# Kernel tuning notes

Hardware: AMD Instinct MI355X
Metric: run time of the kernel (lower is better)

Reference implementation:

```python
import jax, jax.numpy as jnp
import numpy as np

NUM_NODES = 100000
NUM_EDGES = 3200000
NUM_GRAPHS = 64


def gcn_conv(x, edge_index, W, b):
    """PyG GCNConv: add self-loops, symmetric deg normalization, linear, scatter-add."""
    n = x.shape[0]
    loop = jnp.arange(n, dtype=edge_index.dtype)
    src = jnp.concatenate([edge_index[0], loop])  # message sources
    dst = jnp.concatenate([edge_index[1], loop])  # aggregation targets
    deg = jax.ops.segment_sum(jnp.ones_like(src, dtype=x.dtype), dst, num_segments=n)
    dis = jnp.where(deg > 0, jax.lax.rsqrt(jnp.maximum(deg, 1.0)), 0.0)
    norm = dis[src] * dis[dst]  # [E+N]
    h = x @ W  # linear transform first (small dims)
    msg = h[src] * norm[:, None]  # irregular gather
    out = jax.ops.segment_sum(msg, dst, num_segments=n)  # scatter-add
    return out + b


def setup_inputs() -> dict:
    key = jax.random.key(0)
    ks = jax.random.split(key, 12)
    x = jax.random.normal(ks[0], (NUM_NODES, 3), dtype=jnp.float32)
    edge_index = jax.random.randint(ks[1], (2, NUM_EDGES), 0, NUM_NODES, dtype=jnp.int64)
    batch = jnp.sort(jax.random.randint(ks[2], (NUM_NODES,), 0, NUM_GRAPHS, dtype=jnp.int64))
    def glorot(k, fan_in, fan_out):
        s = (6.0 / (fan_in + fan_out)) ** 0.5
        return jax.random.uniform(k, (fan_in, fan_out), jnp.float32, -s, s)
    return {
        'x': x, 'edge_index': edge_index, 'batch': batch,
        'W1': glorot(ks[3], 3, 32), 'b1': jnp.zeros((32,), jnp.float32),
        'W2': glorot(ks[4], 32, 16), 'b2': jnp.zeros((16,), jnp.float32),
        'W3': glorot(ks[5], 16, 8), 'b3': jnp.zeros((8,), jnp.float32),
        'Wf': glorot(ks[6], 8, 3), 'bf': jnp.zeros((3,), jnp.float32),
    }


def reference(x, edge_index, batch, W1, b1, W2, b2, W3, b3, Wf, bf):
    h = jax.nn.relu(gcn_conv(x, edge_index, W1, b1))
    h = jax.nn.relu(gcn_conv(h, edge_index, W2, b2))
    h = jax.nn.relu(gcn_conv(h, edge_index, W3, b3))
    # global mean pool over graphs
    sums = jax.ops.segment_sum(h, batch, num_segments=NUM_GRAPHS)
    cnts = jax.ops.segment_sum(jnp.ones((h.shape[0],), h.dtype), batch, num_segments=NUM_GRAPHS)
    pooled = sums / jnp.maximum(cnts, 1.0)[:, None]
    return pooled @ Wf + bf
```

## Files before the change

kernel.cpp:

```cpp
#include <hip/hip_runtime.h>

constexpr int N_NODES  = 100000;
constexpr int N_EDGES  = 3200000;
constexpr int N_GRAPHS = 64;

constexpr int BSHIFT  = 8;
constexpr int NBINS   = (N_NODES + 255) >> BSHIFT;
constexpr int BIN_CAP = 9216;
constexpr int EPB     = 8192;
constexpr int NB_BIN  = (N_EDGES + EPB - 1) / EPB;


__global__ __launch_bounds__(1024) void bin_kernel(
        const int* __restrict__ src, const int* __restrict__ dst,
        int* __restrict__ bin_cur, int2* __restrict__ binned) {
    __shared__ int hist[NBINS];
    __shared__ int base[NBINS];
    int tid = threadIdx.x;
    int e0 = blockIdx.x * EPB;
    int e1 = min(e0 + EPB, N_EDGES);
    for (int i = tid; i < NBINS; i += 1024) hist[i] = 0;
    __syncthreads();
    for (int e = e0 + tid; e < e1; e += 1024) atomicAdd(&hist[dst[e] >> BSHIFT], 1);
    __syncthreads();
    for (int i = tid; i < NBINS; i += 1024) {
        int h = hist[i];
        base[i] = h ? atomicAdd(&bin_cur[i], h) : 0;
    }
    __syncthreads();
    for (int i = tid; i < NBINS; i += 1024) hist[i] = 0;
    __syncthreads();
    for (int e = e0 + tid; e < e1; e += 1024) {
        int d = dst[e];
        int b = d >> BSHIFT;
        int r = base[b] + atomicAdd(&hist[b], 1);
        if (r < BIN_CAP) binned[(size_t)b * BIN_CAP + r] = make_int2(src[e], d);
    }
}

__global__ void binscan_kernel(const int* __restrict__ bin_cur, int* __restrict__ bin_base,
                               int* __restrict__ rowptr) {
    __shared__ int s[512];
    int t = threadIdx.x;
    int v = (t < NBINS) ? bin_cur[t] : 0;
    s[t] = v;
    __syncthreads();
    for (int o = 1; o < 512; o <<= 1) {
        int x = (t >= o) ? s[t - o] : 0;
        __syncthreads();
        s[t] += x;
        __syncthreads();
    }
    if (t < NBINS) bin_base[t] = s[t] - v;
    if (t == 0) rowptr[N_NODES] = N_EDGES;
}

__global__ __launch_bounds__(1024) void csrbuild_kernel(
        const int2* __restrict__ binned, const int* __restrict__ bin_cur,
        const int* __restrict__ bin_base, int* __restrict__ rowptr,
        float* __restrict__ dis, int* __restrict__ csr) {
    __shared__ int cnt[256];
    __shared__ int lofs[256];
    __shared__ int s[256];
    int b = blockIdx.x;
    int t = threadIdx.x;
    int size  = min(bin_cur[b], BIN_CAP);
    int gbase = bin_base[b];
    const int2* bp = binned + (size_t)b * BIN_CAP;
    if (t < 256) cnt[t] = 0;
    __syncthreads();
    for (int i = t; i < size; i += 1024) atomicAdd(&cnt[bp[i].y & 255], 1);
    __syncthreads();
    if (t < 256) {
        int n = (b << BSHIFT) + t;
        int deg = cnt[t];
        if (n < N_NODES) dis[n] = 1.0f / sqrtf((float)deg + 1.0f);
        s[t] = deg;
    }
    __syncthreads();
    for (int o = 1; o < 256; o <<= 1) {
        int x = 0;
        if (t < 256 && t >= o) x = s[t - o];
        __syncthreads();
        if (t < 256) s[t] += x;
        __syncthreads();
    }
    if (t < 256) {
        int n = (b << BSHIFT) + t;
        int deg = cnt[t];
        int excl = s[t] - deg;
        if (n < N_NODES) rowptr[n] = gbase + excl;
        lofs[t] = excl;
        cnt[t] = 0;
    }
    __syncthreads();
    for (int i = t; i < size; i += 1024) {
        int2 ed = bp[i];
        int ln = ed.y & 255;
        int r = atomicAdd(&cnt[ln], 1);
        csr[gbase + lofs[ln] + r] = ed.x;
    }
}


__global__ void pre1_kernel(const float* __restrict__ x, const float* __restrict__ dis,
                            float* __restrict__ xs) {
    int i = blockIdx.x * blockDim.x + threadIdx.x;
    if (i >= N_NODES) return;
    float d = dis[i];
    float4 v;
    v.x = x[(size_t)i * 3 + 0] * d;
    v.y = x[(size_t)i * 3 + 1] * d;
    v.z = x[(size_t)i * 3 + 2] * d;
    v.w = 0.f;
    *reinterpret_cast<float4*>(&xs[(size_t)i * 4]) = v;
}

template<int F, bool ADD_B, bool RELU>
__global__ void gather_kernel(const float* __restrict__ in, const int* __restrict__ rowptr,
                              const int* __restrict__ csr, const float* __restrict__ dis,
                              const float* __restrict__ b, float* __restrict__ out) {
    constexpr int GPB = 256 / F;
    int tid = threadIdx.x;
    int l = tid & (F - 1);
    int n = blockIdx.x * GPB + (tid / F);
    if (n >= N_NODES) return;
    int beg = rowptr[n], end = rowptr[n + 1];
    float a0 = in[(size_t)n * F + l];
    float a1 = 0.f, a2 = 0.f, a3 = 0.f;
    int k = beg;
    for (; k + 3 < end; k += 4) {
        int s0 = csr[k], s1 = csr[k + 1], s2 = csr[k + 2], s3 = csr[k + 3];
        a0 += in[(size_t)s0 * F + l];
        a1 += in[(size_t)s1 * F + l];
        a2 += in[(size_t)s2 * F + l];
        a3 += in[(size_t)s3 * F + l];
    }
    for (; k < end; ++k) a0 += in[(size_t)csr[k] * F + l];
    float v = ((a0 + a1) + (a2 + a3)) * dis[n];
    if (ADD_B) v += b[l];
    if (RELU) v = fmaxf(v, 0.f);
    out[(size_t)n * F + l] = v;
}

__global__ void lin1_kernel(const float* __restrict__ m, const float* __restrict__ W1,
                            const float* __restrict__ b1, float* __restrict__ h1) {
    int i = blockIdx.x * blockDim.x + threadIdx.x;
    if (i >= N_NODES) return;
    float4 mv = *reinterpret_cast<const float4*>(&m[(size_t)i * 4]);
#pragma unroll
    for (int f = 0; f < 32; ++f) {
        float s = b1[f];
        s = fmaf(mv.x, W1[0 * 32 + f], s);
        s = fmaf(mv.y, W1[1 * 32 + f], s);
        s = fmaf(mv.z, W1[2 * 32 + f], s);
        h1[(size_t)i * 32 + f] = fmaxf(s, 0.f);
    }
}

template<int FIN, int FOUT>
__global__ void lin_pre_kernel(const float* __restrict__ in, const float* __restrict__ W,
                               const float* __restrict__ dis, float* __restrict__ g) {
    int i = blockIdx.x * blockDim.x + threadIdx.x;
    if (i >= N_NODES) return;
    float xin[FIN];
#pragma unroll
    for (int k = 0; k < FIN; ++k) xin[k] = in[(size_t)i * FIN + k];
    float d = dis[i];
#pragma unroll
    for (int f = 0; f < FOUT; ++f) {
        float s = 0.f;
#pragma unroll
        for (int k = 0; k < FIN; ++k) s = fmaf(xin[k], W[k * FOUT + f], s);
        g[(size_t)i * FOUT + f] = s * d;
    }
}


__global__ void pool_kernel(const float* __restrict__ h, const int* __restrict__ batch,
                            float* __restrict__ pool) {
    __shared__ float lsum[N_GRAPHS * 8];
    __shared__ float lcnt[N_GRAPHS];
    int tid = threadIdx.x;
    for (int j = tid; j < N_GRAPHS * 8; j += blockDim.x) lsum[j] = 0.f;
    for (int j = tid; j < N_GRAPHS; j += blockDim.x) lcnt[j] = 0.f;
    __syncthreads();
    int i = blockIdx.x * blockDim.x + tid;
    if (i < N_NODES) {
        int gm = batch[i];
        const float4* hp = reinterpret_cast<const float4*>(&h[(size_t)i * 8]);
        float4 a = hp[0], bq = hp[1];
        atomicAdd(&lsum[gm * 8 + 0], a.x);
        atomicAdd(&lsum[gm * 8 + 1], a.y);
        atomicAdd(&lsum[gm * 8 + 2], a.z);
        atomicAdd(&lsum[gm * 8 + 3], a.w);
        atomicAdd(&lsum[gm * 8 + 4], bq.x);
        atomicAdd(&lsum[gm * 8 + 5], bq.y);
        atomicAdd(&lsum[gm * 8 + 6], bq.z);
        atomicAdd(&lsum[gm * 8 + 7], bq.w);
        atomicAdd(&lcnt[gm], 1.0f);
    }
    __syncthreads();
    for (int idx = tid; idx < N_GRAPHS * 9; idx += blockDim.x) {
        int gm = idx / 9, j = idx % 9;
        if (lcnt[gm] != 0.f) {
            if (j < 8) atomicAdd(&pool[gm * 8 + j], lsum[gm * 8 + j]);
            else       atomicAdd(&pool[512 + gm], lcnt[gm]);
        }
    }
}

__global__ void final_kernel(const float* __restrict__ pool, const float* __restrict__ Wf,
                             const float* __restrict__ bf, float* __restrict__ out) {
    int t = threadIdx.x;
    if (t >= N_GRAPHS * 3) return;
    int gm = t / 3, c = t % 3;
    float cnt = fmaxf(pool[512 + gm], 1.0f);
    float s = 0.f;
#pragma unroll
    for (int f = 0; f < 8; ++f) s = fmaf(pool[gm * 8 + f] / cnt, Wf[f * 3 + c], s);
    out[t] = s + bf[c];
}


extern "C" void kernel_launch(void* const* d_in, const int* in_sizes, int n_in,
                              void* d_out, int out_size, void* d_ws, size_t ws_size,
                              hipStream_t stream) {
    const float* x     = (const float*)d_in[0];
    const int*   ei    = (const int*)d_in[1];
    const int*   batch = (const int*)d_in[2];
    const float* W1 = (const float*)d_in[3];
    const float* b1 = (const float*)d_in[4];
    const float* W2 = (const float*)d_in[5];
    const float* b2 = (const float*)d_in[6];
    const float* W3 = (const float*)d_in[7];
    const float* b3 = (const float*)d_in[8];
    const float* Wf = (const float*)d_in[9];
    const float* bf = (const float*)d_in[10];

    const int* src = ei;
    const int* dst = ei + N_EDGES;

    const int N = N_NODES, E = N_EDGES;

    int*   bin_cur  = (int*)d_ws;
    int*   bin_base = bin_cur + NBINS;
    int*   rowptr   = bin_base + NBINS;
    float* dis      = (float*)(rowptr + N + 2);
    int*   csr      = (int*)(dis + N);
    int2*  binned   = (int2*)(csr + E);
    float* xs       = (float*)binned;
    float* m        = xs + (size_t)4 * N;
    float* h1       = m + (size_t)4 * N;
    float* g        = h1 + (size_t)32 * N;
    float* h2       = g + (size_t)16 * N;
    float* pool     = (float*)(binned + (size_t)NBINS * BIN_CAP);
    float* h3       = xs;

    const int B = 256;
    const int NB_N = (N + B - 1) / B;

    hipMemsetAsync(bin_cur, 0, NBINS * sizeof(int), stream);
    hipMemsetAsync(pool, 0, N_GRAPHS * 9 * sizeof(float), stream);

    bin_kernel<<<NB_BIN, 1024, 0, stream>>>(src, dst, bin_cur, binned);
    binscan_kernel<<<1, 512, 0, stream>>>(bin_cur, bin_base, rowptr);
    csrbuild_kernel<<<NBINS, 1024, 0, stream>>>(binned, bin_cur, bin_base, rowptr, dis, csr);

    pre1_kernel<<<NB_N, B, 0, stream>>>(x, dis, xs);
    gather_kernel<4, false, false><<<(N + 63) / 64, B, 0, stream>>>(xs, rowptr, csr, dis, b1, m);
    lin1_kernel<<<NB_N, B, 0, stream>>>(m, W1, b1, h1);

    lin_pre_kernel<32, 16><<<NB_N, B, 0, stream>>>(h1, W2, dis, g);
    gather_kernel<16, true, true><<<(N + 15) / 16, B, 0, stream>>>(g, rowptr, csr, dis, b2, h2);

    lin_pre_kernel<16, 8><<<NB_N, B, 0, stream>>>(h2, W3, dis, g);
    gather_kernel<8, true, true><<<(N + 31) / 32, B, 0, stream>>>(g, rowptr, csr, dis, b3, h3);

    pool_kernel<<<NB_N, B, 0, stream>>>(h3, batch, pool);
    final_kernel<<<1, 256, 0, stream>>>(pool, Wf, bf, (float*)d_out);
}
```

Before: 202.9 us.

## Pack binned edges, locally sort bins in LDS, split 16-wide gather into halves

The bin kernel now stages each block's edges in shared memory and counting-sorts them by bin, so global writes to the binned buffer are contiguous per bin. Each edge is packed into one int holding the low destination bits and the source index, which halves binned traffic; csrbuild keeps these packed values in registers between its two passes. The 16-feature layer-2 gather is split into two 8-feature gathers over separate arrays, trading an extra pass over the CSR for smaller gathered rows. Nontemporal loads and stores are added throughout. The bin kernel uses a large LDS footprint, which lowers occupancy.

```diff
diff --git a/kernel.cpp b/kernel.cpp
--- a/kernel.cpp
+++ b/kernel.cpp
@@ -4,37 +4,83 @@
 constexpr int N_EDGES  = 3200000;
 constexpr int N_GRAPHS = 64;
 
-constexpr int BSHIFT  = 8;
-constexpr int NBINS   = (N_NODES + 255) >> BSHIFT;
-constexpr int BIN_CAP = 9216;
-constexpr int EPB     = 8192;
-constexpr int NB_BIN  = (N_EDGES + EPB - 1) / EPB;
+constexpr int BSHIFT   = 8;
+constexpr int NBINS    = (N_NODES + 255) >> BSHIFT;
+constexpr int BIN_CAP  = 9216;
+constexpr int SRC_BITS = 17;
+constexpr int SRC_MASK = (1 << SRC_BITS) - 1;
+
+constexpr int NB_BIN = 500;
+constexpr int EPB    = N_EDGES / NB_BIN;
+constexpr int EPT    = (EPB + 1023) / 1024;
+
+typedef float v4f __attribute__((ext_vector_type(4)));
 
 
 __global__ __launch_bounds__(1024) void bin_kernel(
         const int* __restrict__ src, const int* __restrict__ dst,
-        int* __restrict__ bin_cur, int2* __restrict__ binned) {
+        int* __restrict__ bin_cur, int* __restrict__ binned) {
+    __shared__ int pk[EPB];
+    __shared__ unsigned short bn[EPB];
+    __shared__ unsigned short ord[EPB];
     __shared__ int hist[NBINS];
-    __shared__ int base[NBINS];
+    __shared__ int lexcl[NBINS];
+    __shared__ int lofs[NBINS];
+    __shared__ int gofs[NBINS];
+    __shared__ int s512[512];
     int tid = threadIdx.x;
     int e0 = blockIdx.x * EPB;
-    int e1 = min(e0 + EPB, N_EDGES);
     for (int i = tid; i < NBINS; i += 1024) hist[i] = 0;
     __syncthreads();
-    for (int e = e0 + tid; e < e1; e += 1024) atomicAdd(&hist[dst[e] >> BSHIFT], 1);
-    __syncthreads();
-    for (int i = tid; i < NBINS; i += 1024) {
-        int h = hist[i];
-        base[i] = h ? atomicAdd(&bin_cur[i], h) : 0;
-    }
-    __syncthreads();
-    for (int i = tid; i < NBINS; i += 1024) hist[i] = 0;
-    __syncthreads();
-    for (int e = e0 + tid; e < e1; e += 1024) {
-        int d = dst[e];
-        int b = d >> BSHIFT;
-        int r = base[b] + atomicAdd(&hist[b], 1);
-        if (r < BIN_CAP) binned[(size_t)b * BIN_CAP + r] = make_int2(src[e], d);
+#pragma unroll
+    for (int k = 0; k < EPT; ++k) {
+        int i = tid + k * 1024;
+        if (i < EPB) {
+            int d = __builtin_nontemporal_load(&dst[e0 + i]);
+            int s = __builtin_nontemporal_load(&src[e0 + i]);
+            int b = d >> BSHIFT;
+            pk[i] = ((d & 255) << SRC_BITS) | s;
+            bn[i] = (unsigned short)b;
+            atomicAdd(&hist[b], 1);
+        }
+    }
+    __syncthreads();
+    if (tid < 512) s512[tid] = (tid < NBINS) ? hist[tid] : 0;
+    __syncthreads();
+    for (int o = 1; o < 512; o <<= 1) {
+        int x = 0;
+        if (tid < 512 && tid >= o) x = s512[tid - o];
+        __syncthreads();
+        if (tid < 512) s512[tid] += x;
+        __syncthreads();
+    }
+    if (tid < NBINS) {
+        int h = hist[tid];
+        int excl = s512[tid] - h;
+        lexcl[tid] = excl;
+        lofs[tid]  = excl;
+        gofs[tid]  = h ? atomicAdd(&bin_cur[tid], h) : 0;
+    }
+    __syncthreads();
+#pragma unroll
+    for (int k = 0; k < EPT; ++k) {
+        int i = tid + k * 1024;
+        if (i < EPB) {
+            int r = atomicAdd(&lofs[bn[i]], 1);
+            ord[r] = (unsigned short)i;
+        }
+    }
+    __syncthreads();
+#pragma unroll
+    for (int k = 0; k < EPT; ++k) {
+        int i = tid + k * 1024;
+        if (i < EPB) {
+            int j = ord[i];
+            int b = bn[j];
+            int pos = gofs[b] + (i - lexcl[b]);
+            if (pos < BIN_CAP)
+                __builtin_nontemporal_store(pk[j], &binned[(size_t)b * BIN_CAP + pos]);
+        }
     }
 }
 
@@ -56,7 +102,7 @@
 }
 
 __global__ __launch_bounds__(1024) void csrbuild_kernel(
-        const int2* __restrict__ binned, const int* __restrict__ bin_cur,
+        const int* __restrict__ binned, const int* __restrict__ bin_cur,
         const int* __restrict__ bin_base, int* __restrict__ rowptr,
         float* __restrict__ dis, int* __restrict__ csr) {
     __shared__ int cnt[256];
@@ -66,10 +112,16 @@
     int t = threadIdx.x;
     int size  = min(bin_cur[b], BIN_CAP);
     int gbase = bin_base[b];
-    const int2* bp = binned + (size_t)b * BIN_CAP;
+    const int* bp = binned + (size_t)b * BIN_CAP;
     if (t < 256) cnt[t] = 0;
     __syncthreads();
-    for (int i = t; i < size; i += 1024) atomicAdd(&cnt[bp[i].y & 255], 1);
+    int pc[9];
+#pragma unroll
+    for (int k = 0; k < 9; ++k) {
+        int i = t + k * 1024;
+        pc[k] = (i < size) ? __builtin_nontemporal_load(&bp[i]) : -1;
+        if (i < size) atomicAdd(&cnt[pc[k] >> SRC_BITS], 1);
+    }
     __syncthreads();
     if (t < 256) {
         int n = (b << BSHIFT) + t;
@@ -87,18 +139,21 @@
     }
     if (t < 256) {
         int n = (b << BSHIFT) + t;
-        int deg = cnt[t];
-        int excl = s[t] - deg;
+        int excl = s[t] - cnt[t];
         if (n < N_NODES) rowptr[n] = gbase + excl;
         lofs[t] = excl;
         cnt[t] = 0;
     }
     __syncthreads();
-    for (int i = t; i < size; i += 1024) {
-        int2 ed = bp[i];
-        int ln = ed.y & 255;
-        int r = atomicAdd(&cnt[ln], 1);
-        csr[gbase + lofs[ln] + r] = ed.x;
+#pragma unroll
+    for (int k = 0; k < 9; ++k) {
+        int i = t + k * 1024;
+        if (i < size) {
+            int p = pc[k];
+            int ln = p >> SRC_BITS;
+            int r = atomicAdd(&cnt[ln], 1);
+            csr[gbase + lofs[ln] + r] = p & SRC_MASK;
+        }
     }
 }
 
@@ -109,14 +164,14 @@
     if (i >= N_NODES) return;
     float d = dis[i];
     float4 v;
-    v.x = x[(size_t)i * 3 + 0] * d;
-    v.y = x[(size_t)i * 3 + 1] * d;
-    v.z = x[(size_t)i * 3 + 2] * d;
+    v.x = __builtin_nontemporal_load(&x[(size_t)i * 3 + 0]) * d;
+    v.y = __builtin_nontemporal_load(&x[(size_t)i * 3 + 1]) * d;
+    v.z = __builtin_nontemporal_load(&x[(size_t)i * 3 + 2]) * d;
     v.w = 0.f;
     *reinterpret_cast<float4*>(&xs[(size_t)i * 4]) = v;
 }
 
-template<int F, bool ADD_B, bool RELU>
+template<int F, bool ADD_B, bool RELU, bool NT_OUT>
 __global__ void gather_kernel(const float* __restrict__ in, const int* __restrict__ rowptr,
                               const int* __restrict__ csr, const float* __restrict__ dis,
                               const float* __restrict__ b, float* __restrict__ out) {
@@ -130,17 +185,21 @@
     float a1 = 0.f, a2 = 0.f, a3 = 0.f;
     int k = beg;
     for (; k + 3 < end; k += 4) {
-        int s0 = csr[k], s1 = csr[k + 1], s2 = csr[k + 2], s3 = csr[k + 3];
+        int s0 = __builtin_nontemporal_load(&csr[k]);
+        int s1 = __builtin_nontemporal_load(&csr[k + 1]);
+        int s2 = __builtin_nontemporal_load(&csr[k + 2]);
+        int s3 = __builtin_nontemporal_load(&csr[k + 3]);
         a0 += in[(size_t)s0 * F + l];
         a1 += in[(size_t)s1 * F + l];
         a2 += in[(size_t)s2 * F + l];
         a3 += in[(size_t)s3 * F + l];
     }
-    for (; k < end; ++k) a0 += in[(size_t)csr[k] * F + l];
+    for (; k < end; ++k) a0 += in[(size_t)__builtin_nontemporal_load(&csr[k]) * F + l];
     float v = ((a0 + a1) + (a2 + a3)) * dis[n];
     if (ADD_B) v += b[l];
     if (RELU) v = fmaxf(v, 0.f);
-    out[(size_t)n * F + l] = v;
+    if (NT_OUT) __builtin_nontemporal_store(v, &out[(size_t)n * F + l]);
+    else        out[(size_t)n * F + l] = v;
 }
 
 __global__ void lin1_kernel(const float* __restrict__ m, const float* __restrict__ W1,
@@ -158,21 +217,48 @@
     }
 }
 
-template<int FIN, int FOUT>
-__global__ void lin_pre_kernel(const float* __restrict__ in, const float* __restrict__ W,
-                               const float* __restrict__ dis, float* __restrict__ g) {
+__global__ void lin_pre2_kernel(const float* __restrict__ h1, const float* __restrict__ W2,
+                                const float* __restrict__ dis,
+                                float* __restrict__ gA, float* __restrict__ gB) {
     int i = blockIdx.x * blockDim.x + threadIdx.x;
     if (i >= N_NODES) return;
-    float xin[FIN];
-#pragma unroll
-    for (int k = 0; k < FIN; ++k) xin[k] = in[(size_t)i * FIN + k];
+    float xin[32];
+    const v4f* hp = reinterpret_cast<const v4f*>(&h1[(size_t)i * 32]);
+#pragma unroll
+    for (int q = 0; q < 8; ++q) {
+        v4f v = __builtin_nontemporal_load(&hp[q]);
+        xin[q * 4 + 0] = v.x; xin[q * 4 + 1] = v.y;
+        xin[q * 4 + 2] = v.z; xin[q * 4 + 3] = v.w;
+    }
     float d = dis[i];
 #pragma unroll
-    for (int f = 0; f < FOUT; ++f) {
+    for (int f = 0; f < 16; ++f) {
         float s = 0.f;
 #pragma unroll
-        for (int k = 0; k < FIN; ++k) s = fmaf(xin[k], W[k * FOUT + f], s);
-        g[(size_t)i * FOUT + f] = s * d;
+        for (int k = 0; k < 32; ++k) s = fmaf(xin[k], W2[k * 16 + f], s);
+        s *= d;
+        if (f < 8) gA[(size_t)i * 8 + f]       = s;
+        else       gB[(size_t)i * 8 + (f - 8)] = s;
+    }
+}
+
+__global__ void lin_pre3_kernel(const float* __restrict__ h2A, const float* __restrict__ h2B,
+                                const float* __restrict__ W3, const float* __restrict__ dis,
+                                float* __restrict__ g8) {
+    int i = blockIdx.x * blockDim.x + threadIdx.x;
+    if (i >= N_NODES) return;
+    float xin[16];
+#pragma unroll
+    for (int k = 0; k < 8; ++k) xin[k]     = h2A[(size_t)i * 8 + k];
+#pragma unroll
+    for (int k = 0; k < 8; ++k) xin[8 + k] = h2B[(size_t)i * 8 + k];
+    float d = dis[i];
+#pragma unroll
+    for (int f = 0; f < 8; ++f) {
+        float s = 0.f;
+#pragma unroll
+        for (int k = 0; k < 16; ++k) s = fmaf(xin[k], W3[k * 8 + f], s);
+        g8[(size_t)i * 8 + f] = s * d;
     }
 }
 
@@ -248,14 +334,18 @@
     int*   rowptr   = bin_base + NBINS;
     float* dis      = (float*)(rowptr + N + 2);
     int*   csr      = (int*)(dis + N);
-    int2*  binned   = (int2*)(csr + E);
-    float* xs       = (float*)binned;
-    float* m        = xs + (size_t)4 * N;
-    float* h1       = m + (size_t)4 * N;
-    float* g        = h1 + (size_t)32 * N;
-    float* h2       = g + (size_t)16 * N;
-    float* pool     = (float*)(binned + (size_t)NBINS * BIN_CAP);
-    float* h3       = xs;
+    float* act      = (float*)(csr + E);
+    int*   binned   = (int*)act;
+    float* xs  = act;
+    float* m   = act + (size_t)4  * N;
+    float* h1  = act + (size_t)8  * N;
+    float* gA  = act + (size_t)40 * N;
+    float* gB  = act + (size_t)48 * N;
+    float* h2A = h1;
+    float* h2B = h1 + (size_t)8 * N;
+    float* g8  = xs;
+    float* h3  = gA;
+    float* pool = act + (size_t)56 * N;
 
     const int B = 256;
     const int NB_N = (N + B - 1) / B;
@@ -268,14 +358,15 @@
     csrbuild_kernel<<<NBINS, 1024, 0, stream>>>(binned, bin_cur, bin_base, rowptr, dis, csr);
 
     pre1_kernel<<<NB_N, B, 0, stream>>>(x, dis, xs);
-    gather_kernel<4, false, false><<<(N + 63) / 64, B, 0, stream>>>(xs, rowptr, csr, dis, b1, m);
+    gather_kernel<4, false, false, false><<<(N + 63) / 64, B, 0, stream>>>(xs, rowptr, csr, dis, b1, m);
     lin1_kernel<<<NB_N, B, 0, stream>>>(m, W1, b1, h1);
 
-    lin_pre_kernel<32, 16><<<NB_N, B, 0, stream>>>(h1, W2, dis, g);
-    gather_kernel<16, true, true><<<(N + 15) / 16, B, 0, stream>>>(g, rowptr, csr, dis, b2, h2);
-
-    lin_pre_kernel<16, 8><<<NB_N, B, 0, stream>>>(h2, W3, dis, g);
-    gather_kernel<8, true, true><<<(N + 31) / 32, B, 0, stream>>>(g, rowptr, csr, dis, b3, h3);
+    lin_pre2_kernel<<<NB_N, B, 0, stream>>>(h1, W2, dis, gA, gB);
+    gather_kernel<8, true, true, true><<<(N + 31) / 32, B, 0, stream>>>(gA, rowptr, csr, dis, b2,     h2A);
+    gather_kernel<8, true, true, true><<<(N + 31) / 32, B, 0, stream>>>(gB, rowptr, csr, dis, b2 + 8, h2B);
+
+    lin_pre3_kernel<<<NB_N, B, 0, stream>>>(h2A, h2B, W3, dis, g8);
+    gather_kernel<8, true, true, false><<<(N + 31) / 32, B, 0, stream>>>(g8, rowptr, csr, dis, b3, h3);
 
     pool_kernel<<<NB_N, B, 0, stream>>>(h3, batch, pool);
     final_kernel<<<1, 256, 0, stream>>>(pool, Wf, bf, (float*)d_out);
```

After: 262.2 us. 1.29x slower.
